# Performance work log

Measured on AMD Instinct MI355X. Metric: run time of the kernel, lower is better.

The kernel has to match this reference:

```python
import jax, jax.numpy as jnp
import numpy as np

N, U, K, S = 1024, 64, 2, 2        # nodes, rnn_units, max_diffusion_step, num_supports
Q = S * K + 1                       # diffusion matrices (incl. identity)
B, T, H = 64, 12, 12                # batch, seq_len, horizon
IN, OUT, L = 1, 1, 2                # input_dim, output_dim, num_rnn_layers


def setup_inputs() -> dict:
    key = jax.random.key(0)
    ks = jax.random.split(key, 16)

    def glorot(k, shape):
        fan = shape[0] + shape[-1]
        return jax.random.normal(k, shape, jnp.float32) * np.float32(np.sqrt(2.0 / fan))

    # random-walk supports from a random dense adjacency (DCRNN: transpose of D^-1 A)
    adj = jax.random.uniform(ks[0], (N, N), jnp.float32)
    rw = lambda a: a / a.sum(axis=1, keepdims=True)
    supports = jnp.stack([rw(adj).T, rw(adj.T).T])  # (S, N, N)

    inputs = jax.random.normal(ks[1], (B, N * IN, T), jnp.float32)

    p = {}
    i = 2
    for pre, ind in (("enc", IN), ("dec", OUT)):
        for l in range(L):
            f = (ind if l == 0 else U) + U
            p[f"{pre}_gw{l}"] = glorot(ks[i], (Q * f, 2 * U)); i += 1
            p[f"{pre}_gb{l}"] = jnp.ones((2 * U,), jnp.float32)   # GRU gate bias init 1.0
            p[f"{pre}_cw{l}"] = glorot(ks[i], (Q * f, U)); i += 1
            p[f"{pre}_cb{l}"] = jnp.zeros((U,), jnp.float32)
    p["proj_w"] = glorot(ks[i], (U, OUT))
    p["proj_b"] = jnp.zeros((OUT,), jnp.float32)
    return {"inputs": inputs, "supports": supports, **p}


def _diffusion(x, supports):
    # x: (B, N, F) -> (B, N, Q*F); Chebyshev-style recurrence as in DCGRUCell._gconv
    mats = [x]
    for s in range(S):
        A = supports[s]
        x0 = x
        x1 = jnp.einsum('nm,bmf->bnf', A, x0)
        mats.append(x1)
        for _ in range(2, K + 1):
            x2 = 2.0 * jnp.einsum('nm,bmf->bnf', A, x1) - x0
            mats.append(x2)
            x0, x1 = x1, x2
    return jnp.concatenate(mats, axis=-1)


def _cell(x, h, supports, gw, gb, cw, cb):
    # x: (B,N,Fin), h: (B,N,U)
    ru = jax.nn.sigmoid(_diffusion(jnp.concatenate([x, h], -1), supports) @ gw + gb)
    r, u = ru[..., :U], ru[..., U:]
    c = jnp.tanh(_diffusion(jnp.concatenate([x, r * h], -1), supports) @ cw + cb)
    return u * h + (1.0 - u) * c


def reference(inputs, supports,
              enc_gw0, enc_gb0, enc_cw0, enc_cb0,
              enc_gw1, enc_gb1, enc_cw1, enc_cb1,
              dec_gw0, dec_gb0, dec_cw0, dec_cb0,
              dec_gw1, dec_gb1, dec_cw1, dec_cb1,
              proj_w, proj_b):
    enc = [(enc_gw0, enc_gb0, enc_cw0, enc_cb0), (enc_gw1, enc_gb1, enc_cw1, enc_cb1)]
    dec = [(dec_gw0, dec_gb0, dec_cw0, dec_cb0), (dec_gw1, dec_gb1, dec_cw1, dec_cb1)]

    x_seq = inputs.reshape(B, N, IN, T).transpose(3, 0, 1, 2)  # (T, B, N, IN)
    h0 = jnp.zeros((L, B, N, U), inputs.dtype)

    def enc_step(h, x):
        out, hs = x, []
        for l in range(L):
            hn = _cell(out, h[l], supports, *enc[l])
            hs.append(hn)
            out = hn
        return jnp.stack(hs), None

    hT, _ = jax.lax.scan(enc_step, h0, x_seq)

    def dec_step(carry, _):
        h, xin = carry
        out, hs = xin, []
        for l in range(L):
            hn = _cell(out, h[l], supports, *dec[l])
            hs.append(hn)
            out = hn
        proj = out @ proj_w + proj_b          # (B, N, OUT)
        return (jnp.stack(hs), proj), proj.reshape(B, N * OUT)

    go = jnp.zeros((B, N, OUT), inputs.dtype)
    _, outs = jax.lax.scan(dec_step, (hT, go), None, length=H)
    return outs  # (H, B, N*OUT)
```

## Files before the change

### kernel.cpp

```cpp
#include <hip/hip_runtime.h>

typedef _Float16 f16;
typedef _Float16 f16x4 __attribute__((ext_vector_type(4)));
typedef _Float16 f16x8 __attribute__((ext_vector_type(8)));
typedef float    f32x4 __attribute__((ext_vector_type(4)));

#define NN 1024
#define NT 12
#define NHOR 12
#define ROWS (NN*64)
#define MATH (1024*1024)
static const long SLOT = (long)NN*4096;

__device__ __forceinline__ int sw4(int row){ return (row ^ (row>>2)) & 3; }

__device__ __forceinline__ int ilvpos(int k){
  int r = k & 31;
  return (k & ~31) + ((r & 12) << 1) + (r & 3) + ((r & 16) >> 2);
}

template<int NR>
__device__ __forceinline__ void stage(f16* lds, const f16* src, int ldk, int k0, int tid){
  #pragma unroll
  for (int ic=0; ic<NR/64; ++ic){
    const int c = tid + ic*256;
    const int row = c>>2, c4 = c&3;
    const f16* g = src + (long)row*ldk + k0 + ((c4 ^ sw4(row))<<3);
    f16* d = lds + c*8;
    __builtin_amdgcn_global_load_lds((const __attribute__((address_space(1))) void*)g,
                                     (__attribute__((address_space(3))) void*)d, 16, 0, 0);
  }
}

__device__ __forceinline__ f16x8 fragI(const f16* lds, int row, int rq){
  return *(const f16x8*)&lds[row*32 + ((rq ^ sw4(row))<<3)];
}

__device__ __forceinline__ f16x8 fragN(const f16* lds, int row, int lk){
  const int s = sw4(row);
  const int cl = (lk>>3) ^ s, ch = (2|(lk>>3)) ^ s;
  f16x4 lo = *(const f16x4*)&lds[row*32 + (cl<<3) + (lk&7)];
  f16x4 hi = *(const f16x4*)&lds[row*32 + (ch<<3) + (lk&7)];
  f16x8 r; r[0]=lo[0];r[1]=lo[1];r[2]=lo[2];r[3]=lo[3];
  r[4]=hi[0];r[5]=hi[1];r[6]=hi[2];r[7]=hi[3];
  return r;
}

struct DiffP {
  const f16* A0; const f16* A1;
  const f16* B;
  f16* out0; f16* out1;
  int nt0;
  int a0tr, a1tr;
  int mode_x;
  int wsq;
};

__global__ __launch_bounds__(256) void gemm_diff(DiffP p) {
  __shared__ f16 As[128*32];
  __shared__ f16 Bs[128*32];
  const int tid=threadIdx.x, l=tid&63, w=tid>>6;
  const int rq=l>>4, ro=l&15, lk=rq*4;
  const int rt=blockIdx.x, ct=blockIdx.y;
  const int part = (rt >= p.nt0);
  const int rtl  = part ? (rt - p.nt0) : rt;
  const int atr  = part ? p.a1tr : p.a0tr;
  const f16* Ab  = part ? p.A1 : p.A0;
  const f16* Bbase = p.B + (long)ct*128*1024;
  const int wm=(w>>1)*64, wc=(w&1)*64;
  const int n_t  = ((tid>>5)&1)*16 + ((tid>>3)&3)*4 + ((tid>>1)&3);
  const int but0 = ((tid>>6)&3)*16 + (tid&1)*8;
  const f16* gtr = Ab + (long)n_t*4096 + (long)rtl*128 + but0;
  const f16* Ailv = Ab + (long)rtl*128*1024;
  f32x4 acc[4][4] = {};
  for (int k0=0; k0<1024; k0+=32) {
    if (atr) {
      const f16* g = gtr + (long)k0*4096;
      __builtin_amdgcn_global_load_lds((const __attribute__((address_space(1))) void*)g,
                                       (__attribute__((address_space(3))) void*)(As + tid*8), 16, 0, 0);
      __builtin_amdgcn_global_load_lds((const __attribute__((address_space(1))) void*)(g + 64),
                                       (__attribute__((address_space(3))) void*)(As + (tid+256)*8), 16, 0, 0);
    } else {
      stage<128>(As, Ailv, 1024, k0, tid);
    }
    stage<128>(Bs, Bbase, 1024, k0, tid);
    __syncthreads();
    f16x8 a[4], b[4];
    if (atr) {
      const unsigned abase = (unsigned)(size_t)(__attribute__((address_space(3))) f16*)&As[0]
                           + (unsigned)((w>>1)*4096 + l*8);
      f16x4 tlo[4], thi[4];
      #pragma unroll
      for (int i=0;i<4;i++){
        asm volatile("ds_read_b64_tr_b16 %0, %1 offset:%2" : "=v"(tlo[i]) : "v"(abase), "i"(i*1024));
        asm volatile("ds_read_b64_tr_b16 %0, %1 offset:%2" : "=v"(thi[i]) : "v"(abase), "i"(i*1024+512));
      }
      asm volatile("s_waitcnt lgkmcnt(0)" ::: "memory");
      __builtin_amdgcn_sched_barrier(0);
      #pragma unroll
      for (int i=0;i<4;i++){
        f16x8 t2; t2[0]=tlo[i][0];t2[1]=tlo[i][1];t2[2]=tlo[i][2];t2[3]=tlo[i][3];
        t2[4]=thi[i][0];t2[5]=thi[i][1];t2[6]=thi[i][2];t2[7]=thi[i][3];
        a[i]=t2;
      }
    } else {
      #pragma unroll
      for (int i=0;i<4;i++) a[i] = fragI(As, wm + i*16 + ro, rq);
    }
    #pragma unroll
    for (int j=0;j<4;j++) b[j] = fragI(Bs, wc + j*16 + ro, rq);
    #pragma unroll
    for (int i=0;i<4;i++)
      #pragma unroll
      for (int j=0;j<4;j++)
        acc[i][j] = __builtin_amdgcn_mfma_f32_16x16x32_f16(b[j], a[i], acc[i][j], 0,0,0);
    __syncthreads();
  }
  if (p.wsq) {
    #pragma unroll
    for (int i=0;i<4;i++){
      const long rg = (long)rt*128 + wm + i*16 + ro;
      #pragma unroll
      for (int j=0;j<4;j++){
        const int cb = ct*128 + wc + j*16 + lk;
        f16x4 sv;
        #pragma unroll
        for (int e=0;e<4;e++) sv[e] = (f16)(2.f*acc[i][j][e] - ((rg==(long)(cb+e))?1.f:0.f));
        *(f16x4*)&p.out0[rg*1024 + cb] = sv;
      }
    }
    return;
  }
  f16* ob = part ? p.out1 : p.out0;
  const int mode = part ? p.mode_x : 0;
  const long rowbase = (long)rtl*128;
  #pragma unroll
  for (int i=0;i<4;i++){
    const int bu = wm + i*16 + ro;
    if (mode==2 && bu>=64) continue;
    #pragma unroll
    for (int j=0;j<4;j++){
      const int cb = ct*128 + wc + j*16 + lk;
      #pragma unroll
      for (int e=0;e<4;e++){
        const int c = cb + e, q = c>>10, n = c&1023;
        const f16 v = (f16)acc[i][j][e];
        if (mode==0) ob[(long)q*SLOT + (long)n*4096 + rowbase + bu] = v;
        else         ob[(long)q*ROWS + n*64 + bu] = v;
      }
    }
  }
}

struct Tab5 { const f16* p[5]; };
struct CellP {
  Tab5 ta, tb, xq;
  const f16 *wa, *wb, *wx0;
  const float* bias;
  const float* h32in;
  f16* rh; float* u32;
  float* h32io; f16* h16io;
  int nseg, xf1;
};

template<int O, int GATE>
__global__ __launch_bounds__(256) void cell_gemm(CellP p) {
  constexpr int FC = O/32;
  __shared__ f16 As[128*32];
  __shared__ f16 Bs[O*32];
  const int tid=threadIdx.x, l=tid&63, w=tid>>6;
  const int rq=l>>4, ro=l&15, lk=rq*4;
  const int wm=(w>>1)*64, wc=(w&1)*(O/2);
  f32x4 acc[4][FC] = {};
  const long r0 = (long)blockIdx.x*128;
  const int Ktot = p.nseg*320;
  for (int kg=0; kg<Ktot; kg+=32) {
    const int seg = (kg>=320) ? 1 : 0;
    const int kk  = kg - seg*320;
    const int q = kk>>6, kq = kk&63;
    const f16* asrc = (seg ? p.tb.p[q] : p.ta.p[q]) + r0*64;
    const f16* wsrc = seg ? p.wb : p.wa;
    stage<128>(As, asrc, 64, kq, tid);
    stage<O>(Bs, wsrc, 320, kk, tid);
    __syncthreads();
    f16x8 a[4], b[FC];
    #pragma unroll
    for (int i=0;i<4;i++) a[i] = fragN(As, wm + i*16 + ro, lk);
    #pragma unroll
    for (int j=0;j<FC;j++) b[j] = fragI(Bs, wc + j*16 + ro, rq);
    #pragma unroll
    for (int i=0;i<4;i++)
      #pragma unroll
      for (int j=0;j<FC;j++)
        acc[i][j] = __builtin_amdgcn_mfma_f32_16x16x32_f16(a[i], b[j], acc[i][j], 0,0,0);
    __syncthreads();
  }
  #pragma unroll
  for (int i=0;i<4;i++) {
    #pragma unroll
    for (int e=0;e<4;e++) {
      const long rg = r0 + wm + i*16 + rq*4 + e;
      float xv[5];
      if (p.xf1) {
        #pragma unroll
        for (int q2=0;q2<5;q2++) xv[q2] = (float)p.xq.p[q2][rg];
      }
      #pragma unroll
      for (int j=0;j<FC;j++) {
        const int col = wc + j*16 + ro;
        float v = acc[i][j][e] + p.bias[col];
        if (p.xf1) {
          #pragma unroll
          for (int q2=0;q2<5;q2++) v += xv[q2] * (float)p.wx0[q2*O + col];
        }
        if (GATE) {
          const float s = 1.f/(1.f + __expf(-v));
          if (col < 64) p.rh[rg*64 + col] = (f16)(s * p.h32in[rg*64 + col]);
          else          p.u32[rg*64 + (col-64)] = s;
        } else {
          const float cc = tanhf(v);
          const float u  = p.u32[rg*64 + col];
          const float h  = p.h32io[rg*64 + col];
          const float hn = u*h + (1.f-u)*cc;
          p.h32io[rg*64 + col] = hn;
          p.h16io[rg*64 + col] = (f16)hn;
        }
      }
    }
  }
}

__global__ __launch_bounds__(256) void k_transpose(const f16* in, f16* out, int R, int C) {
  __shared__ f16 T[64*66];
  const long rb = (long)blockIdx.x*64, cb = (long)blockIdx.y*64;
  const int t = threadIdx.x;
  #pragma unroll
  for (int it=0; it<2; ++it) {
    const int r = (t>>3) + it*32, c8 = (t&7)*8;
    f16x8 v = *(const f16x8*)(in + (rb+r)*C + cb + c8);
    *(f16x8*)&T[r*66 + c8] = v;
  }
  __syncthreads();
  #pragma unroll
  for (int it=0; it<2; ++it) {
    const int c = (t>>3) + it*32, r8 = (t&7)*8;
    f16x8 v;
    #pragma unroll
    for (int j=0;j<8;j++) v[j] = T[(r8+j)*66 + c];
    *(f16x8*)(out + (cb+c)*R + rb + r8) = v;
  }
}

__global__ void k_cast_sup(const float* s, f16* o) {
  long i = (long)blockIdx.x*256 + threadIdx.x;
  if (i < 2LL*MATH) o[i] = (f16)s[i];
}

__global__ void k_ilv(const f16* in, f16* out) {
  int i = blockIdx.x*256 + threadIdx.x;
  if (i >= MATH) return;
  int r = i>>10, k = i&1023;
  out[(long)r*1024 + ilvpos(k)] = in[i];
}

__global__ void k_pack_x(const float* in, f16* xe, f16* xet) {
  int i = blockIdx.x*256 + threadIdx.x;
  if (i >= NT*ROWS) return;
  int t = i / ROWS, r = i % ROWS, n = r>>6, b = r&63;
  float v = in[(long)b*NN*NT + (long)n*NT + t];
  xe[i] = (f16)v;
  xet[(long)t*131072 + (long)b*1024 + ilvpos(n)] = (f16)v;
}

__global__ void k_split_w_t(const float* src, f16* wh_t, f16* wxA, int f, int xf, int O) {
  int i = blockIdx.x*256 + threadIdx.x;
  if (i >= 5*f*O) return;
  int o = i % O, rr = i / O, q = rr / f, ff = rr % f;
  f16 v = (f16)src[i];
  if (ff < xf) {
    if (xf == 1) wxA[q*O + o] = v;
    else         wxA[(long)o*320 + q*64 + ilvpos(ff)] = v;
  } else {
    wh_t[(long)o*320 + q*64 + ilvpos(ff - xf)] = v;
  }
}

__global__ void k_proj(const float* h32, const float* pw, const float* pb,
                       float* out, f16* xdec, f16* xdect) {
  int r = blockIdx.x*256 + threadIdx.x;
  if (r >= ROWS) return;
  float acc = pb[0];
  const float* hp = h32 + (long)r*64;
  #pragma unroll
  for (int k=0;k<64;k++) acc += hp[k]*pw[k];
  int n = r>>6, b = r&63;
  out[(long)b*NN + n] = acc;
  xdec[r] = (f16)acc;
  xdect[(long)b*1024 + ilvpos(n)] = (f16)acc;
}

extern "C" void kernel_launch(void* const* d_in, const int* in_sizes, int n_in,
                              void* d_out, int out_size, void* d_ws, size_t ws_size,
                              hipStream_t stream) {
  (void)in_sizes; (void)n_in; (void)out_size; (void)ws_size;
  const float* inputs = (const float*)d_in[0];
  const float* sup    = (const float*)d_in[1];
  const float* gwp[4] = {(const float*)d_in[2], (const float*)d_in[6], (const float*)d_in[10], (const float*)d_in[14]};
  const float* gbp[4] = {(const float*)d_in[3], (const float*)d_in[7], (const float*)d_in[11], (const float*)d_in[15]};
  const float* cwp[4] = {(const float*)d_in[4], (const float*)d_in[8], (const float*)d_in[12], (const float*)d_in[16]};
  const float* cbp[4] = {(const float*)d_in[5], (const float*)d_in[9], (const float*)d_in[13], (const float*)d_in[17]};
  const float* pw = (const float*)d_in[18];
  const float* pb = (const float*)d_in[19];
  float* out = (float*)d_out;

  char* base = (char*)d_ws; size_t off = 0;
  auto alloc = [&](size_t bytes)->void* { void* p = base + off; off += (bytes + 255) & ~(size_t)255; return p; };
  f16* W16int = (f16*)alloc(4LL*MATH*2);
  f16* xenc   = (f16*)alloc((long)NT*ROWS*2);
  f16* xet    = (f16*)alloc((long)NT*131072*2);
  f16* xdec   = (f16*)alloc((long)ROWS*2);
  f16* xdect  = (f16*)alloc(131072L*2);
  f16*  h16[2]  = {(f16*)alloc((long)ROWS*64*2),  (f16*)alloc((long)ROWS*64*2)};
  float* h32[2] = {(float*)alloc((long)ROWS*64*4), (float*)alloc((long)ROWS*64*4)};
  float* u32 = (float*)alloc((long)ROWS*64*4);
  f16* rh    = (f16*)alloc((long)ROWS*64*2);
  f16* Dh    = (f16*)alloc(4*SLOT*2);
  f16* Dx    = (f16*)alloc(4*SLOT*2);
  f16* Dx0   = (f16*)alloc(4LL*ROWS*2);
  f16 *gwh[4], *gwx[4], *cwh[4], *cwx[4];
  for (int i=0;i<4;i++) {
    gwh[i]=(f16*)alloc(128L*320*2); gwx[i]=(f16*)alloc(128L*320*2);
    cwh[i]=(f16*)alloc(64L*320*2);  cwx[i]=(f16*)alloc(64L*320*2);
  }

  hipMemsetAsync(h16[0], 0, (long)ROWS*64*2, stream);
  hipMemsetAsync(h16[1], 0, (long)ROWS*64*2, stream);
  hipMemsetAsync(h32[0], 0, (long)ROWS*64*4, stream);
  hipMemsetAsync(h32[1], 0, (long)ROWS*64*4, stream);
  hipMemsetAsync(xdec,   0, (long)ROWS*2, stream);
  hipMemsetAsync(xdect,  0, 131072L*2, stream);

  f16* tmpA   = Dh;
  f16* tmpAt  = Dh + 2L*MATH;
  f16* tmpAti = Dh + 4L*MATH;
  f16* tmpSq  = Dh + 5L*MATH;
  k_cast_sup<<<(2*MATH+255)/256, 256, 0, stream>>>(sup, tmpA);
  for (int s=0;s<2;s++) {
    k_transpose<<<dim3(16,16),256,0,stream>>>(tmpA + (long)s*MATH, tmpAt + (long)s*MATH, 1024, 1024);
    k_ilv<<<4096,256,0,stream>>>(tmpA + (long)s*MATH, W16int + (long)(2*s)*MATH);
  }
  for (int s=0;s<2;s++) {
    k_ilv<<<4096,256,0,stream>>>(tmpAt + (long)s*MATH, tmpAti);
    DiffP mp{};
    mp.A0 = W16int + (long)(2*s)*MATH; mp.A1 = mp.A0; mp.a0tr = 0; mp.a1tr = 0; mp.nt0 = 8;
    mp.B = tmpAti; mp.out0 = tmpSq; mp.wsq = 1;
    gemm_diff<<<dim3(8,8),256,0,stream>>>(mp);
    k_ilv<<<4096,256,0,stream>>>(tmpSq, W16int + (long)(2*s+1)*MATH);
  }
  k_pack_x<<<(NT*ROWS+255)/256,256,0,stream>>>(inputs, xenc, xet);
  const int fs[4]  = {65,128,65,128};
  const int xfs[4] = {1,64,1,64};
  for (int i=0;i<4;i++) {
    k_split_w_t<<<(5*fs[i]*128+255)/256,256,0,stream>>>(gwp[i], gwh[i], gwx[i], fs[i], xfs[i], 128);
    k_split_w_t<<<(5*fs[i]*64 +255)/256,256,0,stream>>>(cwp[i], cwh[i], cwx[i], fs[i], xfs[i], 64);
  }

  auto run_cell = [&](const f16* xraw, const f16* xA, int xf,
                      f16* h16c, float* h32c, int wi) {
    DiffP dp{};
    dp.A0 = h16c; dp.a0tr = 1; dp.nt0 = 32; dp.B = W16int; dp.out0 = Dh; dp.wsq = 0;
    int gx;
    if (xf == 64) { dp.A1 = xA; dp.a1tr = 1; dp.out1 = Dx;  dp.mode_x = 0; gx = 64; }
    else          { dp.A1 = xA; dp.a1tr = 0; dp.out1 = Dx0; dp.mode_x = 2; gx = 33; }
    gemm_diff<<<dim3(gx, 32), 256, 0, stream>>>(dp);
    CellP gp{};
    gp.ta.p[0] = h16c; for (int q=1;q<5;q++) gp.ta.p[q] = Dh + (long)(q-1)*SLOT;
    gp.wa = gwh[wi]; gp.bias = gbp[wi];
    gp.h32in = h32c; gp.rh = rh; gp.u32 = u32;
    if (xf == 64) {
      gp.nseg = 2; gp.xf1 = 0;
      gp.tb.p[0] = xraw; for (int q=1;q<5;q++) gp.tb.p[q] = Dx + (long)(q-1)*SLOT;
      gp.wb = gwx[wi];
    } else {
      gp.nseg = 1; gp.xf1 = 1;
      gp.xq.p[0] = xraw; for (int q=1;q<5;q++) gp.xq.p[q] = Dx0 + (long)(q-1)*ROWS;
      gp.wx0 = gwx[wi];
    }
    cell_gemm<128,1><<<512, 256, 0, stream>>>(gp);
    DiffP dp2{};
    dp2.A0 = rh; dp2.a0tr = 1; dp2.A1 = rh; dp2.a1tr = 1; dp2.nt0 = 32;
    dp2.B = W16int; dp2.out0 = Dh; dp2.wsq = 0;
    gemm_diff<<<dim3(32, 32), 256, 0, stream>>>(dp2);
    CellP cp{};
    cp.ta.p[0] = rh; for (int q=1;q<5;q++) cp.ta.p[q] = Dh + (long)(q-1)*SLOT;
    cp.wa = cwh[wi]; cp.bias = cbp[wi];
    cp.u32 = u32; cp.h32io = h32c; cp.h16io = h16c;
    if (xf == 64) {
      cp.nseg = 2; cp.xf1 = 0;
      cp.tb.p[0] = xraw; for (int q=1;q<5;q++) cp.tb.p[q] = Dx + (long)(q-1)*SLOT;
      cp.wb = cwx[wi];
    } else {
      cp.nseg = 1; cp.xf1 = 1;
      cp.xq.p[0] = xraw; for (int q=1;q<5;q++) cp.xq.p[q] = Dx0 + (long)(q-1)*ROWS;
      cp.wx0 = cwx[wi];
    }
    cell_gemm<64,0><<<512, 256, 0, stream>>>(cp);
  };

  for (int t=0;t<NT;t++) {
    run_cell(xenc + (long)t*ROWS, xet + (long)t*131072, 1, h16[0], h32[0], 0);
    run_cell(h16[0], h16[0],                           64, h16[1], h32[1], 1);
  }
  for (int s=0;s<NHOR;s++) {
    run_cell(xdec,   xdect,   1, h16[0], h32[0], 2);
    run_cell(h16[0], h16[0], 64, h16[1], h32[1], 3);
    k_proj<<<ROWS/256, 256, 0, stream>>>(h32[1], pw, pb, out + (long)s*ROWS, xdec, xdect);
  }
}
```

Measured before the change: 11.00 ms.

## Emit pre-transposed hidden states from cell epilogues and double-buffer GEMM LDS

The cell epilogues now also write the r*h and new-h states into a transposed, interleaved (batch*unit, node) layout. The diffusion GEMM can then load its activation operand with the plain swizzled staging path, dropping the ds_read_b64_tr transposed load and swapping the grid roles of the W and Y operands. Both the diffusion GEMM and the cell GEMM double-buffer their LDS tiles so the next K-slice's global-to-LDS loads overlap the current MFMAs. The cost is extra scattered f16 stores in the epilogues, twice the LDS per block, and two more full-size state buffers.

Result: slower. 12.61 ms (+14.6%).

```diff
diff --git a/kernel.cpp b/kernel.cpp
--- a/kernel.cpp
+++ b/kernel.cpp
@@ -26,9 +26,8 @@
     const int c = tid + ic*256;
     const int row = c>>2, c4 = c&3;
     const f16* g = src + (long)row*ldk + k0 + ((c4 ^ sw4(row))<<3);
-    f16* d = lds + c*8;
     __builtin_amdgcn_global_load_lds((const __attribute__((address_space(1))) void*)g,
-                                     (__attribute__((address_space(3))) void*)d, 16, 0, 0);
+                                     (__attribute__((address_space(3))) void*)(lds + c*8), 16, 0, 0);
   }
 }
 
@@ -47,74 +46,55 @@
 }
 
 struct DiffP {
-  const f16* A0; const f16* A1;
-  const f16* B;
+  const f16* W;
+  const f16* Y0; const f16* Y1;
   f16* out0; f16* out1;
-  int nt0;
-  int a0tr, a1tr;
+  int nct0;
   int mode_x;
   int wsq;
 };
 
 __global__ __launch_bounds__(256) void gemm_diff(DiffP p) {
-  __shared__ f16 As[128*32];
-  __shared__ f16 Bs[128*32];
+  __shared__ f16 Ws[2][128*32];
+  __shared__ f16 Ys[2][128*32];
   const int tid=threadIdx.x, l=tid&63, w=tid>>6;
   const int rq=l>>4, ro=l&15, lk=rq*4;
   const int rt=blockIdx.x, ct=blockIdx.y;
-  const int part = (rt >= p.nt0);
-  const int rtl  = part ? (rt - p.nt0) : rt;
-  const int atr  = part ? p.a1tr : p.a0tr;
-  const f16* Ab  = part ? p.A1 : p.A0;
-  const f16* Bbase = p.B + (long)ct*128*1024;
+  const int part = (ct >= p.nct0);
+  const int ctl  = part ? (ct - p.nct0) : ct;
+  const f16* Wb = p.W + (long)rt*128*1024;
+  const f16* Yb = (part ? p.Y1 : p.Y0) + (long)ctl*128*1024;
   const int wm=(w>>1)*64, wc=(w&1)*64;
-  const int n_t  = ((tid>>5)&1)*16 + ((tid>>3)&3)*4 + ((tid>>1)&3);
-  const int but0 = ((tid>>6)&3)*16 + (tid&1)*8;
-  const f16* gtr = Ab + (long)n_t*4096 + (long)rtl*128 + but0;
-  const f16* Ailv = Ab + (long)rtl*128*1024;
   f32x4 acc[4][4] = {};
-  for (int k0=0; k0<1024; k0+=32) {
-    if (atr) {
-      const f16* g = gtr + (long)k0*4096;
-      __builtin_amdgcn_global_load_lds((const __attribute__((address_space(1))) void*)g,
-                                       (__attribute__((address_space(3))) void*)(As + tid*8), 16, 0, 0);
-      __builtin_amdgcn_global_load_lds((const __attribute__((address_space(1))) void*)(g + 64),
-                                       (__attribute__((address_space(3))) void*)(As + (tid+256)*8), 16, 0, 0);
+  stage<128>(Ws[0], Wb, 1024, 0, tid);
+  stage<128>(Ys[0], Yb, 1024, 0, tid);
+  __syncthreads();
+  int cur = 0;
+  for (int t=0; t<32; ++t) {
+    if (t<31) {
+      stage<128>(Ws[cur^1], Wb, 1024, (t+1)*32, tid);
+      stage<128>(Ys[cur^1], Yb, 1024, (t+1)*32, tid);
+    }
+    f16x8 wf[4], yf[4];
+    #pragma unroll
+    for (int i=0;i<4;i++) wf[i] = fragI(Ws[cur], wm + i*16 + ro, rq);
+    #pragma unroll
+    for (int j=0;j<4;j++) yf[j] = fragI(Ys[cur], wc + j*16 + ro, rq);
+    if (!p.wsq) {
+      #pragma unroll
+      for (int i=0;i<4;i++)
+        #pragma unroll
+        for (int j=0;j<4;j++)
+          acc[i][j] = __builtin_amdgcn_mfma_f32_16x16x32_f16(wf[i], yf[j], acc[i][j], 0,0,0);
     } else {
-      stage<128>(As, Ailv, 1024, k0, tid);
-    }
-    stage<128>(Bs, Bbase, 1024, k0, tid);
+      #pragma unroll
+      for (int i=0;i<4;i++)
+        #pragma unroll
+        for (int j=0;j<4;j++)
+          acc[i][j] = __builtin_amdgcn_mfma_f32_16x16x32_f16(yf[j], wf[i], acc[i][j], 0,0,0);
+    }
     __syncthreads();
-    f16x8 a[4], b[4];
-    if (atr) {
-      const unsigned abase = (unsigned)(size_t)(__attribute__((address_space(3))) f16*)&As[0]
-                           + (unsigned)((w>>1)*4096 + l*8);
-      f16x4 tlo[4], thi[4];
-      #pragma unroll
-      for (int i=0;i<4;i++){
-        asm volatile("ds_read_b64_tr_b16 %0, %1 offset:%2" : "=v"(tlo[i]) : "v"(abase), "i"(i*1024));
-        asm volatile("ds_read_b64_tr_b16 %0, %1 offset:%2" : "=v"(thi[i]) : "v"(abase), "i"(i*1024+512));
-      }
-      asm volatile("s_waitcnt lgkmcnt(0)" ::: "memory");
-      __builtin_amdgcn_sched_barrier(0);
-      #pragma unroll
-      for (int i=0;i<4;i++){
-        f16x8 t2; t2[0]=tlo[i][0];t2[1]=tlo[i][1];t2[2]=tlo[i][2];t2[3]=tlo[i][3];
-        t2[4]=thi[i][0];t2[5]=thi[i][1];t2[6]=thi[i][2];t2[7]=thi[i][3];
-        a[i]=t2;
-      }
-    } else {
-      #pragma unroll
-      for (int i=0;i<4;i++) a[i] = fragI(As, wm + i*16 + ro, rq);
-    }
-    #pragma unroll
-    for (int j=0;j<4;j++) b[j] = fragI(Bs, wc + j*16 + ro, rq);
-    #pragma unroll
-    for (int i=0;i<4;i++)
-      #pragma unroll
-      for (int j=0;j<4;j++)
-        acc[i][j] = __builtin_amdgcn_mfma_f32_16x16x32_f16(b[j], a[i], acc[i][j], 0,0,0);
-    __syncthreads();
+    cur ^= 1;
   }
   if (p.wsq) {
     #pragma unroll
@@ -133,20 +113,18 @@
   }
   f16* ob = part ? p.out1 : p.out0;
   const int mode = part ? p.mode_x : 0;
-  const long rowbase = (long)rtl*128;
   #pragma unroll
   for (int i=0;i<4;i++){
-    const int bu = wm + i*16 + ro;
-    if (mode==2 && bu>=64) continue;
-    #pragma unroll
-    for (int j=0;j<4;j++){
-      const int cb = ct*128 + wc + j*16 + lk;
-      #pragma unroll
-      for (int e=0;e<4;e++){
-        const int c = cb + e, q = c>>10, n = c&1023;
+    #pragma unroll
+    for (int e=0;e<4;e++){
+      const int c = rt*128 + wm + i*16 + rq*4 + e;
+      const int q = c>>10, n = c&1023;
+      #pragma unroll
+      for (int j=0;j<4;j++){
+        const int bul = wc + j*16 + ro;
         const f16 v = (f16)acc[i][j][e];
-        if (mode==0) ob[(long)q*SLOT + (long)n*4096 + rowbase + bu] = v;
-        else         ob[(long)q*ROWS + n*64 + bu] = v;
+        if (mode==0) ob[(long)q*SLOT + (long)n*4096 + (long)ctl*128 + bul] = v;
+        else if (bul < 64) ob[(long)q*ROWS + n*64 + bul] = v;
       }
     }
   }
@@ -158,48 +136,57 @@
   const f16 *wa, *wb, *wx0;
   const float* bias;
   const float* h32in;
-  f16* rh; float* u32;
-  float* h32io; f16* h16io;
+  f16* rh; f16* rhhat; float* u32;
+  float* h32io; f16* h16io; f16* hhat;
   int nseg, xf1;
 };
 
 template<int O, int GATE>
 __global__ __launch_bounds__(256) void cell_gemm(CellP p) {
   constexpr int FC = O/32;
-  __shared__ f16 As[128*32];
-  __shared__ f16 Bs[O*32];
+  __shared__ f16 As[2][128*32];
+  __shared__ f16 Bs[2][O*32];
   const int tid=threadIdx.x, l=tid&63, w=tid>>6;
   const int rq=l>>4, ro=l&15, lk=rq*4;
   const int wm=(w>>1)*64, wc=(w&1)*(O/2);
   f32x4 acc[4][FC] = {};
   const long r0 = (long)blockIdx.x*128;
-  const int Ktot = p.nseg*320;
-  for (int kg=0; kg<Ktot; kg+=32) {
-    const int seg = (kg>=320) ? 1 : 0;
-    const int kk  = kg - seg*320;
+  const int nt = p.nseg*10;
+  auto stg = [&](int buf, int t){
+    const int kg = t*32;
+    const int seg = (kg>=320)?1:0;
+    const int kk = kg - seg*320;
     const int q = kk>>6, kq = kk&63;
     const f16* asrc = (seg ? p.tb.p[q] : p.ta.p[q]) + r0*64;
     const f16* wsrc = seg ? p.wb : p.wa;
-    stage<128>(As, asrc, 64, kq, tid);
-    stage<O>(Bs, wsrc, 320, kk, tid);
-    __syncthreads();
+    stage<128>(As[buf], asrc, 64, kq, tid);
+    stage<O>(Bs[buf], wsrc, 320, kk, tid);
+  };
+  stg(0,0);
+  __syncthreads();
+  int cur = 0;
+  for (int t=0; t<nt; ++t) {
+    if (t+1<nt) stg(cur^1, t+1);
     f16x8 a[4], b[FC];
     #pragma unroll
-    for (int i=0;i<4;i++) a[i] = fragN(As, wm + i*16 + ro, lk);
-    #pragma unroll
-    for (int j=0;j<FC;j++) b[j] = fragI(Bs, wc + j*16 + ro, rq);
+    for (int i=0;i<4;i++) a[i] = fragN(As[cur], wm + i*16 + ro, lk);
+    #pragma unroll
+    for (int j=0;j<FC;j++) b[j] = fragI(Bs[cur], wc + j*16 + ro, rq);
     #pragma unroll
     for (int i=0;i<4;i++)
       #pragma unroll
       for (int j=0;j<FC;j++)
         acc[i][j] = __builtin_amdgcn_mfma_f32_16x16x32_f16(a[i], b[j], acc[i][j], 0,0,0);
     __syncthreads();
+    cur ^= 1;
   }
   #pragma unroll
   for (int i=0;i<4;i++) {
     #pragma unroll
     for (int e=0;e<4;e++) {
       const long rg = r0 + wm + i*16 + rq*4 + e;
+      const int bb = (int)(rg & 63), nn2 = (int)(rg >> 6);
+      const long hcol = (long)ilvpos(nn2);
       float xv[5];
       if (p.xf1) {
         #pragma unroll
@@ -215,8 +202,13 @@
         }
         if (GATE) {
           const float s = 1.f/(1.f + __expf(-v));
-          if (col < 64) p.rh[rg*64 + col] = (f16)(s * p.h32in[rg*64 + col]);
-          else          p.u32[rg*64 + (col-64)] = s;
+          if (col < 64) {
+            const float rhv = s * p.h32in[rg*64 + col];
+            p.rh[rg*64 + col] = (f16)rhv;
+            p.rhhat[((long)bb*64 + col)*1024 + hcol] = (f16)rhv;
+          } else {
+            p.u32[rg*64 + (col-64)] = s;
+          }
         } else {
           const float cc = tanhf(v);
           const float u  = p.u32[rg*64 + col];
@@ -224,6 +216,7 @@
           const float hn = u*h + (1.f-u)*cc;
           p.h32io[rg*64 + col] = hn;
           p.h16io[rg*64 + col] = (f16)hn;
+          p.hhat[((long)bb*64 + col)*1024 + hcol] = (f16)hn;
         }
       }
     }
@@ -321,9 +314,11 @@
   f16* xdec   = (f16*)alloc((long)ROWS*2);
   f16* xdect  = (f16*)alloc(131072L*2);
   f16*  h16[2]  = {(f16*)alloc((long)ROWS*64*2),  (f16*)alloc((long)ROWS*64*2)};
+  f16*  hh[2]   = {(f16*)alloc(4096L*1024*2),     (f16*)alloc(4096L*1024*2)};
   float* h32[2] = {(float*)alloc((long)ROWS*64*4), (float*)alloc((long)ROWS*64*4)};
   float* u32 = (float*)alloc((long)ROWS*64*4);
   f16* rh    = (f16*)alloc((long)ROWS*64*2);
+  f16* rhh   = (f16*)alloc(4096L*1024*2);
   f16* Dh    = (f16*)alloc(4*SLOT*2);
   f16* Dx    = (f16*)alloc(4*SLOT*2);
   f16* Dx0   = (f16*)alloc(4LL*ROWS*2);
@@ -335,6 +330,8 @@
 
   hipMemsetAsync(h16[0], 0, (long)ROWS*64*2, stream);
   hipMemsetAsync(h16[1], 0, (long)ROWS*64*2, stream);
+  hipMemsetAsync(hh[0],  0, 4096L*1024*2, stream);
+  hipMemsetAsync(hh[1],  0, 4096L*1024*2, stream);
   hipMemsetAsync(h32[0], 0, (long)ROWS*64*4, stream);
   hipMemsetAsync(h32[1], 0, (long)ROWS*64*4, stream);
   hipMemsetAsync(xdec,   0, (long)ROWS*2, stream);
@@ -352,8 +349,8 @@
   for (int s=0;s<2;s++) {
     k_ilv<<<4096,256,0,stream>>>(tmpAt + (long)s*MATH, tmpAti);
     DiffP mp{};
-    mp.A0 = W16int + (long)(2*s)*MATH; mp.A1 = mp.A0; mp.a0tr = 0; mp.a1tr = 0; mp.nt0 = 8;
-    mp.B = tmpAti; mp.out0 = tmpSq; mp.wsq = 1;
+    mp.W = W16int + (long)(2*s)*MATH; mp.Y0 = tmpAti; mp.Y1 = tmpAti;
+    mp.out0 = tmpSq; mp.nct0 = 8; mp.wsq = 1;
     gemm_diff<<<dim3(8,8),256,0,stream>>>(mp);
     k_ilv<<<4096,256,0,stream>>>(tmpSq, W16int + (long)(2*s+1)*MATH);
   }
@@ -365,18 +362,18 @@
     k_split_w_t<<<(5*fs[i]*64 +255)/256,256,0,stream>>>(cwp[i], cwh[i], cwx[i], fs[i], xfs[i], 64);
   }
 
-  auto run_cell = [&](const f16* xraw, const f16* xA, int xf,
-                      f16* h16c, float* h32c, int wi) {
+  auto run_cell = [&](const f16* xraw, const f16* xhat, int xf,
+                      f16* h16c, f16* hhatc, float* h32c, int wi) {
     DiffP dp{};
-    dp.A0 = h16c; dp.a0tr = 1; dp.nt0 = 32; dp.B = W16int; dp.out0 = Dh; dp.wsq = 0;
-    int gx;
-    if (xf == 64) { dp.A1 = xA; dp.a1tr = 1; dp.out1 = Dx;  dp.mode_x = 0; gx = 64; }
-    else          { dp.A1 = xA; dp.a1tr = 0; dp.out1 = Dx0; dp.mode_x = 2; gx = 33; }
-    gemm_diff<<<dim3(gx, 32), 256, 0, stream>>>(dp);
+    dp.W = W16int; dp.Y0 = hhatc; dp.out0 = Dh; dp.nct0 = 32; dp.wsq = 0;
+    int gy;
+    if (xf == 64) { dp.Y1 = xhat; dp.out1 = Dx;  dp.mode_x = 0; gy = 64; }
+    else          { dp.Y1 = xhat; dp.out1 = Dx0; dp.mode_x = 2; gy = 33; }
+    gemm_diff<<<dim3(32, gy), 256, 0, stream>>>(dp);
     CellP gp{};
     gp.ta.p[0] = h16c; for (int q=1;q<5;q++) gp.ta.p[q] = Dh + (long)(q-1)*SLOT;
     gp.wa = gwh[wi]; gp.bias = gbp[wi];
-    gp.h32in = h32c; gp.rh = rh; gp.u32 = u32;
+    gp.h32in = h32c; gp.rh = rh; gp.rhhat = rhh; gp.u32 = u32;
     if (xf == 64) {
       gp.nseg = 2; gp.xf1 = 0;
       gp.tb.p[0] = xraw; for (int q=1;q<5;q++) gp.tb.p[q] = Dx + (long)(q-1)*SLOT;
@@ -388,13 +385,12 @@
     }
     cell_gemm<128,1><<<512, 256, 0, stream>>>(gp);
     DiffP dp2{};
-    dp2.A0 = rh; dp2.a0tr = 1; dp2.A1 = rh; dp2.a1tr = 1; dp2.nt0 = 32;
-    dp2.B = W16int; dp2.out0 = Dh; dp2.wsq = 0;
+    dp2.W = W16int; dp2.Y0 = rhh; dp2.Y1 = rhh; dp2.out0 = Dh; dp2.nct0 = 32; dp2.wsq = 0;
     gemm_diff<<<dim3(32, 32), 256, 0, stream>>>(dp2);
     CellP cp{};
     cp.ta.p[0] = rh; for (int q=1;q<5;q++) cp.ta.p[q] = Dh + (long)(q-1)*SLOT;
     cp.wa = cwh[wi]; cp.bias = cbp[wi];
-    cp.u32 = u32; cp.h32io = h32c; cp.h16io = h16c;
+    cp.u32 = u32; cp.h32io = h32c; cp.h16io = h16c; cp.hhat = hhatc;
     if (xf == 64) {
       cp.nseg = 2; cp.xf1 = 0;
       cp.tb.p[0] = xraw; for (int q=1;q<5;q++) cp.tb.p[q] = Dx + (long)(q-1)*SLOT;
@@ -408,12 +404,12 @@
   };
 
   for (int t=0;t<NT;t++) {
-    run_cell(xenc + (long)t*ROWS, xet + (long)t*131072, 1, h16[0], h32[0], 0);
-    run_cell(h16[0], h16[0],                           64, h16[1], h32[1], 1);
+    run_cell(xenc + (long)t*ROWS, xet + (long)t*131072, 1, h16[0], hh[0], h32[0], 0);
+    run_cell(h16[0], hh[0],                            64, h16[1], hh[1], h32[1], 1);
   }
   for (int s=0;s<NHOR;s++) {
-    run_cell(xdec,   xdect,   1, h16[0], h32[0], 2);
-    run_cell(h16[0], h16[0], 64, h16[1], h32[1], 3);
+    run_cell(xdec,   xdect,   1, h16[0], hh[0], h32[0], 2);
+    run_cell(h16[0], hh[0],  64, h16[1], hh[1], h32[1], 3);
     k_proj<<<ROWS/256, 256, 0, stream>>>(h32[1], pw, pb, out + (long)s*ROWS, xdec, xdect);
   }
 }
```
